# Performance work log

Hardware: AMD Instinct MI355X
Metric: run time of the kernel (lower is better)

The kernel has to match this reference:

```python
import jax, jax.numpy as jnp
import numpy as np

IN_F = 256
OUT_F = 256
ALPHA = 0.2  # LeakyReLU negative slope


def _xavier(key, shape, gain=1.414):
    fan_in, fan_out = shape[0], shape[1]
    limit = gain * np.sqrt(6.0 / (fan_in + fan_out))
    return jax.random.uniform(key, shape, jnp.float32, -limit, limit)


def setup_inputs() -> dict:
    key = jax.random.key(0)
    k1, k2, k3, k4, k5, k6 = jax.random.split(key, 6)
    B, N = 8, 2048
    h = jax.random.normal(k1, (B, N, IN_F), jnp.float32)
    adj = jax.random.randint(k2, (B, N, N), 0, 2, jnp.int32)
    lrgt1 = jax.random.normal(k3, (B, N, OUT_F), jnp.float32)
    W1 = _xavier(k4, (IN_F, IN_F))
    W2 = _xavier(k5, (OUT_F, OUT_F))
    a = _xavier(k6, (2 * IN_F, 1))
    return {"h": h, "adj": adj, "lrgt1": lrgt1, "W1": W1, "W2": W2, "a": a}


def reference(h, adj, lrgt1, W1, W2, a):
    # Wh: [B,N,in], wlrgt: [B,N,out]
    Wh = jnp.matmul(h, W1)
    wlrgt = jnp.matmul(lrgt1, W2)
    # additive attention scores: e[b,i,j] = leaky_relu(Wh_i @ a1 + Wh_j @ a2)
    a1 = a[:IN_F, 0]   # [in]
    a2 = a[IN_F:, 0]   # [in]
    Wh1 = jnp.einsum('bnc,c->bn', Wh, a1)  # [B,N]
    Wh2 = jnp.einsum('bnc,c->bn', Wh, a2)  # [B,N]
    e = jax.nn.leaky_relu(Wh1[:, :, None] + Wh2[:, None, :], ALPHA)  # [B,N,N]
    neg = jnp.float32(-9e15)
    masked = jnp.where(adj > 0, e, neg)
    attention = jax.nn.softmax(masked, axis=2)
    # dropout p=0.0 / eval mode -> identity
    h_prime = jnp.matmul(attention, Wh)      # [B,N,in]
    gt_prime = jnp.matmul(attention, wlrgt)  # [B,N,out]
    return (jax.nn.elu(h_prime), jax.nn.elu(gt_prime))
```

## Files before the change

### kernel.cpp

```cpp
#include <hip/hip_runtime.h>
#include <hip/hip_bf16.h>

#define IN_F 256
#define NN   2048
#define BB   8
#define NEGV (-9.0e15f)

typedef unsigned short u16;
typedef __attribute__((ext_vector_type(8))) short short8x;
typedef __attribute__((ext_vector_type(4))) float float4x;

__device__ __forceinline__ u16 f2b(float f) {
    union { float f; unsigned int u; } x; x.f = f;
    unsigned int r = x.u + 0x7FFFu + ((x.u >> 16) & 1u);
    return (u16)(r >> 16);
}

__device__ __forceinline__ float logitf(float wh1v, float w, int av) {
    float e = wh1v + w;
    e = (e >= 0.f) ? e : 0.2f * e;
    return (av > 0) ? e : NEGV;
}

__device__ __forceinline__ void transp_body(const float* __restrict__ src,
                                            u16* __restrict__ dst,
                                            int R, int C, int tid,
                                            float (*tile)[33])
{
    const int per = (R / 32) * (C / 32);
    const int b  = tid / per;
    const int tt = tid % per;
    const int jt = tt / (C / 32);
    const int ct = tt % (C / 32);
    src += (long)b * R * C;
    dst += (long)b * R * C;

    const int tx = threadIdx.x & 31, ty = threadIdx.x >> 5;
#pragma unroll
    for (int i = 0; i < 4; ++i)
        tile[ty + i * 8][tx] = src[(long)(jt * 32 + ty + i * 8) * C + ct * 32 + tx];
    __syncthreads();
#pragma unroll
    for (int i = 0; i < 4; ++i)
        dst[(long)(ct * 32 + ty + i * 8) * R + jt * 32 + tx] = f2b(tile[tx][ty + i * 8]);
}

__global__ __launch_bounds__(256) void prep(const float* __restrict__ h,
                                            const float* __restrict__ g,
                                            const float* __restrict__ W1,
                                            const float* __restrict__ W2,
                                            const float* __restrict__ a,
                                            u16* __restrict__ HbfT,
                                            u16* __restrict__ GbfT,
                                            u16* __restrict__ W1T,
                                            u16* __restrict__ W2T,
                                            float* __restrict__ v1,
                                            float* __restrict__ v2)
{
    __shared__ float tile[32][33];
    __shared__ float s1[IN_F], s2[IN_F];
    const int bid = blockIdx.x;

    if (bid < 4096) {
        transp_body(h, HbfT, NN, IN_F, bid, tile);
    } else if (bid < 8192) {
        transp_body(g, GbfT, NN, IN_F, bid - 4096, tile);
    } else if (bid < 8256) {
        transp_body(W1, W1T, IN_F, IN_F, bid - 8192, tile);
    } else if (bid < 8320) {
        transp_body(W2, W2T, IN_F, IN_F, bid - 8256, tile);
    } else {
        const int t = threadIdx.x;
        s1[t] = a[t];
        s2[t] = a[IN_F + t];
        __syncthreads();
        float acc1 = 0.f, acc2 = 0.f;
        for (int c = 0; c < IN_F; ++c) {
            float w = W1[t * IN_F + c];
            acc1 += w * s1[c];
            acc2 += w * s2[c];
        }
        v1[t] = acc1;
        v2[t] = acc2;
    }
}

__global__ __launch_bounds__(256) void rowdots(const float* __restrict__ h,
                                               const float* __restrict__ v1,
                                               const float* __restrict__ v2,
                                               float* __restrict__ Wh1,
                                               float* __restrict__ Wh2)
{
    const int wave = threadIdx.x >> 6;
    const int lane = threadIdx.x & 63;
    const long row = (long)blockIdx.x * 4 + wave;
    const int c0 = lane * 4;

    float4 v  = *(const float4*)(h + row * IN_F + c0);
    float4 a1 = *(const float4*)(v1 + c0);
    float4 a2 = *(const float4*)(v2 + c0);

    float s1 = v.x * a1.x + v.y * a1.y + v.z * a1.z + v.w * a1.w;
    float s2 = v.x * a2.x + v.y * a2.y + v.z * a2.z + v.w * a2.w;
#pragma unroll
    for (int off = 32; off; off >>= 1) {
        s1 += __shfl_xor(s1, off, 64);
        s2 += __shfl_xor(s2, off, 64);
    }
    if (lane == 0) { Wh1[row] = s1; Wh2[row] = s2; }
}

__global__ __launch_bounds__(512, 4) void attn_mfma(
    const int* __restrict__ adj,
    const u16* __restrict__ HbfT, const u16* __restrict__ GbfT,
    const float* __restrict__ Wh1, const float* __restrict__ Wh2,
    u16* __restrict__ PH, u16* __restrict__ PG)
{
    const int t = threadIdx.x;
    const int wave = t >> 6, lane = t & 63;
    const int b = blockIdx.x >> 6;
    const long gi0 = (long)blockIdx.x * 32;

    __shared__ __align__(16) u16 Afrag[2][4096];
    __shared__ float sred[512];
    __shared__ float ssc[33];

    const int rr = t >> 4, sg = t & 15;
    const long adjR = (gi0 + rr) * (long)NN;
    const float* wh2b = Wh2 + (long)b * NN;
    const float wh1rr = Wh1[gi0 + rr];

    {
        float4 w = *(const float4*)(wh2b + t * 4);
        sred[t] = fmaxf(fmaxf(w.x, w.y), fmaxf(w.z, w.w));
    }
    __syncthreads();
    if (t < 64) {
        float v = sred[t * 8];
#pragma unroll
        for (int k = 1; k < 8; ++k) v = fmaxf(v, sred[t * 8 + k]);
#pragma unroll
        for (int off = 32; off; off >>= 1) v = fmaxf(v, __shfl_xor(v, off, 64));
        if (t == 0) ssc[32] = v;
    }
    __syncthreads();
    const float mm = wh1rr + ssc[32];
    const float mv = (mm >= 0.f) ? mm : 0.2f * mm;

    const int ks0 = sg >> 2;
    const int wl  = (rr & 15) + ((sg & 3) << 4);
    const int prt = rr >> 4;
    const int aoff = ((ks0 * 2 + prt) * 64 + wl) * 8;

    float4x accH[2][2], accG[2][2];
#pragma unroll
    for (int rt = 0; rt < 2; ++rt)
#pragma unroll
        for (int ct = 0; ct < 2; ++ct) {
            accH[rt][ct] = (float4x)0.0f;
            accG[rt][ct] = (float4x)0.0f;
        }

    const int bn = lane & 15, bq = lane >> 4;
    const long hbase = (long)b * IN_F * NN;
    float lloc = 0.f;

    int4   a0 = *(const int4*)(adj + adjR + sg * 8);
    int4   a1 = *(const int4*)(adj + adjR + sg * 8 + 4);
    float4 w0 = *(const float4*)(wh2b + sg * 8);
    float4 w1 = *(const float4*)(wh2b + sg * 8 + 4);

    for (int kch = 0; kch < 16; ++kch) {
        const int j0 = kch * 128;

        union { short8x v; u16 u[8]; } pk;
        float p;
        p = __expf(logitf(wh1rr, w0.x, a0.x) - mv); lloc += p; pk.u[0] = f2b(p);
        p = __expf(logitf(wh1rr, w0.y, a0.y) - mv); lloc += p; pk.u[1] = f2b(p);
        p = __expf(logitf(wh1rr, w0.z, a0.z) - mv); lloc += p; pk.u[2] = f2b(p);
        p = __expf(logitf(wh1rr, w0.w, a0.w) - mv); lloc += p; pk.u[3] = f2b(p);
        p = __expf(logitf(wh1rr, w1.x, a1.x) - mv); lloc += p; pk.u[4] = f2b(p);
        p = __expf(logitf(wh1rr, w1.y, a1.y) - mv); lloc += p; pk.u[5] = f2b(p);
        p = __expf(logitf(wh1rr, w1.z, a1.z) - mv); lloc += p; pk.u[6] = f2b(p);
        p = __expf(logitf(wh1rr, w1.w, a1.w) - mv); lloc += p; pk.u[7] = f2b(p);

        if (kch < 15) {
            const long o = adjR + (kch + 1) * 128 + sg * 8;
            const int  w = (kch + 1) * 128 + sg * 8;
            a0 = *(const int4*)(adj + o);
            a1 = *(const int4*)(adj + o + 4);
            w0 = *(const float4*)(wh2b + w);
            w1 = *(const float4*)(wh2b + w + 4);
        }

        *(short8x*)&Afrag[kch & 1][aoff] = pk.v;
        __syncthreads();

        const u16* ab = Afrag[kch & 1];
#pragma unroll
        for (int ks = 0; ks < 4; ++ks) {
            short8x A0 = *(const short8x*)&ab[((ks * 2 + 0) * 64 + lane) * 8];
            short8x A1 = *(const short8x*)&ab[((ks * 2 + 1) * 64 + lane) * 8];
            const int jj = j0 + ks * 32 + bq * 8;
#pragma unroll
            for (int ct = 0; ct < 2; ++ct) {
                const int c = wave * 32 + ct * 16 + bn;
                const long bi = hbase + (long)c * NN + jj;
                short8x Bh = *(const short8x*)(HbfT + bi);
                short8x Bg = *(const short8x*)(GbfT + bi);
                accH[0][ct] = __builtin_amdgcn_mfma_f32_16x16x32_bf16(A0, Bh, accH[0][ct], 0, 0, 0);
                accH[1][ct] = __builtin_amdgcn_mfma_f32_16x16x32_bf16(A1, Bh, accH[1][ct], 0, 0, 0);
                accG[0][ct] = __builtin_amdgcn_mfma_f32_16x16x32_bf16(A0, Bg, accG[0][ct], 0, 0, 0);
                accG[1][ct] = __builtin_amdgcn_mfma_f32_16x16x32_bf16(A1, Bg, accG[1][ct], 0, 0, 0);
            }
        }
    }

    __syncthreads();
    sred[rr * 16 + sg] = lloc;
    __syncthreads();
    if (t < 32) {
        float v = sred[t * 16];
#pragma unroll
        for (int k = 1; k < 16; ++k) v += sred[t * 16 + k];
        ssc[t] = 1.0f / v;
    }
    __syncthreads();

#pragma unroll
    for (int rt = 0; rt < 2; ++rt)
#pragma unroll
        for (int ct = 0; ct < 2; ++ct) {
            const int c = wave * 32 + ct * 16 + bn;
#pragma unroll
            for (int reg = 0; reg < 4; ++reg) {
                const int rl = rt * 16 + bq * 4 + reg;
                const float il = ssc[rl];
                const long row = gi0 + rl;
                PH[row * IN_F + c] = f2b(accH[rt][ct][reg] * il);
                PG[row * IN_F + c] = f2b(accG[rt][ct][reg] * il);
            }
        }
}

__global__ __launch_bounds__(256) void epi2(const u16* __restrict__ PH,
                                            const u16* __restrict__ PG,
                                            const u16* __restrict__ W1T,
                                            const u16* __restrict__ W2T,
                                            float* __restrict__ out)
{
    int bid = blockIdx.x;
    const u16* X;
    const u16* WT;
    float* o;
    if (bid < 512) { X = PH; WT = W1T; o = out; }
    else           { X = PG; WT = W2T; o = out + (long)BB * NN * IN_F; bid -= 512; }

    const int t = threadIdx.x;
    const int wave = t >> 6, lane = t & 63;
    const long i0 = (long)bid * 32;

    __shared__ __align__(16) u16 Afrag[8 * 2 * 64 * 8];

    const int m = t >> 3, ks0 = t & 7, rt0 = m >> 4, lm = m & 15;
    const u16* xp = X + (i0 + m) * IN_F + ks0 * 32;
#pragma unroll
    for (int q = 0; q < 4; ++q) {
        short8x v = *(const short8x*)(xp + q * 8);
        *(short8x*)&Afrag[((ks0 * 2 + rt0) * 64 + lm + q * 16) * 8] = v;
    }
    __syncthreads();

    float4x acc[2][4];
#pragma unroll
    for (int rt = 0; rt < 2; ++rt)
#pragma unroll
        for (int ct = 0; ct < 4; ++ct) acc[rt][ct] = (float4x)0.0f;

    const int bn = lane & 15, bq = lane >> 4;
#pragma unroll
    for (int ks = 0; ks < 8; ++ks) {
        short8x A0 = *(const short8x*)&Afrag[((ks * 2 + 0) * 64 + lane) * 8];
        short8x A1 = *(const short8x*)&Afrag[((ks * 2 + 1) * 64 + lane) * 8];
#pragma unroll
        for (int ct = 0; ct < 4; ++ct) {
            const int n = wave * 64 + ct * 16 + bn;
            short8x Bw = *(const short8x*)(WT + n * IN_F + ks * 32 + bq * 8);
            acc[0][ct] = __builtin_amdgcn_mfma_f32_16x16x32_bf16(A0, Bw, acc[0][ct], 0, 0, 0);
            acc[1][ct] = __builtin_amdgcn_mfma_f32_16x16x32_bf16(A1, Bw, acc[1][ct], 0, 0, 0);
        }
    }

#pragma unroll
    for (int rt = 0; rt < 2; ++rt)
#pragma unroll
        for (int ct = 0; ct < 4; ++ct) {
            const int n = wave * 64 + ct * 16 + bn;
#pragma unroll
            for (int reg = 0; reg < 4; ++reg) {
                const long row = i0 + rt * 16 + bq * 4 + reg;
                float v = acc[rt][ct][reg];
                v = (v > 0.f) ? v : (__expf(v) - 1.f);
                o[row * IN_F + n] = v;
            }
        }
}

extern "C" void kernel_launch(void* const* d_in, const int* in_sizes, int n_in,
                              void* d_out, int out_size, void* d_ws, size_t ws_size,
                              hipStream_t stream)
{
    int ih = -1, ig = -1, iadj = -1, iw1 = -1, iw2 = -1, ia = -1;
    for (int i = 0; i < n_in; ++i) {
        int s = in_sizes[i];
        if      (s == BB * NN * NN)   { if (iadj < 0) iadj = i; }
        else if (s == BB * NN * IN_F) { if (ih < 0) ih = i; else if (ig < 0) ig = i; }
        else if (s == IN_F * IN_F)    { if (iw1 < 0) iw1 = i; else if (iw2 < 0) iw2 = i; }
        else if (s == 2 * IN_F)       { if (ia < 0) ia = i; }
    }
    if (ih < 0 || ig < 0 || iadj < 0 || iw1 < 0 || iw2 < 0 || ia < 0) {
        ih = 0; iadj = 1; ig = 2; iw1 = 3; iw2 = 4; ia = 5;
    }
    const float* h     = (const float*)d_in[ih];
    const int*   adj   = (const int*)  d_in[iadj];
    const float* lrgt1 = (const float*)d_in[ig];
    const float* W1    = (const float*)d_in[iw1];
    const float* W2    = (const float*)d_in[iw2];
    const float* a     = (const float*)d_in[ia];
    float* out = (float*)d_out;

    float* ws   = (float*)d_ws;
    float* v1   = ws;
    float* v2   = v1 + IN_F;
    float* Wh1  = v2 + IN_F;
    float* Wh2  = Wh1 + BB * NN;
    u16* W1T  = (u16*)(Wh2 + BB * NN);
    u16* W2T  = W1T + IN_F * IN_F;
    u16* HbfT = W2T + IN_F * IN_F;
    u16* GbfT = HbfT + (long)BB * IN_F * NN;
    u16* PH   = GbfT + (long)BB * IN_F * NN;
    u16* PG   = PH + (long)BB * NN * IN_F;

    const int nrows = BB * NN;

    prep     <<<8321,        256, 0, stream>>>(h, lrgt1, W1, W2, a,
                                               HbfT, GbfT, W1T, W2T, v1, v2);
    rowdots  <<<nrows / 4,   256, 0, stream>>>(h, v1, v2, Wh1, Wh2);
    attn_mfma<<<nrows / 32,  512, 0, stream>>>(adj, HbfT, GbfT, Wh1, Wh2, PH, PG);
    epi2     <<<2 * nrows / 32, 256, 0, stream>>>(PH, PG, W1T, W2T, out);
}
```

Measured before the change: 364.1 us.

## Software-pipeline B operand loads, swizzle block order, and lighten barrier

Register-prefetches the next k-step's B fragments (H and G, both column tiles) one step ahead so global load latency overlaps the current MFMAs. Swizzles the block index so consecutive workgroups come from different batches. Replaces __syncthreads with an explicit lgkmcnt wait plus s_barrier, so pending global prefetches are not drained at the barrier. This costs extra vector registers for the prefetched fragments, and the swizzle changes how L2 is shared between blocks.

Measured after the change: 375.6 us. 3.1% more time.

```diff
diff --git a/kernel.cpp b/kernel.cpp
--- a/kernel.cpp
+++ b/kernel.cpp
@@ -118,8 +118,9 @@
 {
     const int t = threadIdx.x;
     const int wave = t >> 6, lane = t & 63;
-    const int b = blockIdx.x >> 6;
-    const long gi0 = (long)blockIdx.x * 32;
+    const int bswz = ((blockIdx.x & 7) << 6) | (blockIdx.x >> 3);
+    const int b = bswz >> 6;
+    const long gi0 = (long)bswz * 32;
 
     __shared__ __align__(16) u16 Afrag[2][4096];
     __shared__ float sred[512];
@@ -165,10 +166,20 @@
     const long hbase = (long)b * IN_F * NN;
     float lloc = 0.f;
 
+    const u16* Hb0 = HbfT + hbase + (long)(wave * 32 + bn) * NN;
+    const u16* Hb1 = Hb0 + 16 * (long)NN;
+    const u16* Gb0 = GbfT + hbase + (long)(wave * 32 + bn) * NN;
+    const u16* Gb1 = Gb0 + 16 * (long)NN;
+
     int4   a0 = *(const int4*)(adj + adjR + sg * 8);
     int4   a1 = *(const int4*)(adj + adjR + sg * 8 + 4);
     float4 w0 = *(const float4*)(wh2b + sg * 8);
     float4 w1 = *(const float4*)(wh2b + sg * 8 + 4);
+
+    short8x Bc0 = *(const short8x*)(Hb0 + bq * 8);
+    short8x Bc1 = *(const short8x*)(Gb0 + bq * 8);
+    short8x Bc2 = *(const short8x*)(Hb1 + bq * 8);
+    short8x Bc3 = *(const short8x*)(Gb1 + bq * 8);
 
     for (int kch = 0; kch < 16; ++kch) {
         const int j0 = kch * 128;
@@ -194,25 +205,31 @@
         }
 
         *(short8x*)&Afrag[kch & 1][aoff] = pk.v;
-        __syncthreads();
+        asm volatile("s_waitcnt lgkmcnt(0)\n\ts_barrier" ::: "memory");
 
         const u16* ab = Afrag[kch & 1];
+        const int jb = j0 + bq * 8;
 #pragma unroll
         for (int ks = 0; ks < 4; ++ks) {
             short8x A0 = *(const short8x*)&ab[((ks * 2 + 0) * 64 + lane) * 8];
             short8x A1 = *(const short8x*)&ab[((ks * 2 + 1) * 64 + lane) * 8];
-            const int jj = j0 + ks * 32 + bq * 8;
-#pragma unroll
-            for (int ct = 0; ct < 2; ++ct) {
-                const int c = wave * 32 + ct * 16 + bn;
-                const long bi = hbase + (long)c * NN + jj;
-                short8x Bh = *(const short8x*)(HbfT + bi);
-                short8x Bg = *(const short8x*)(GbfT + bi);
-                accH[0][ct] = __builtin_amdgcn_mfma_f32_16x16x32_bf16(A0, Bh, accH[0][ct], 0, 0, 0);
-                accH[1][ct] = __builtin_amdgcn_mfma_f32_16x16x32_bf16(A1, Bh, accH[1][ct], 0, 0, 0);
-                accG[0][ct] = __builtin_amdgcn_mfma_f32_16x16x32_bf16(A0, Bg, accG[0][ct], 0, 0, 0);
-                accG[1][ct] = __builtin_amdgcn_mfma_f32_16x16x32_bf16(A1, Bg, accG[1][ct], 0, 0, 0);
-            }
+            const int jn = (ks < 3) ? (jb + (ks + 1) * 32)
+                                    : ((kch < 15) ? (jb + 128) : jb);
+            short8x Bn0 = *(const short8x*)(Hb0 + jn);
+            short8x Bn1 = *(const short8x*)(Gb0 + jn);
+            short8x Bn2 = *(const short8x*)(Hb1 + jn);
+            short8x Bn3 = *(const short8x*)(Gb1 + jn);
+
+            accH[0][0] = __builtin_amdgcn_mfma_f32_16x16x32_bf16(A0, Bc0, accH[0][0], 0, 0, 0);
+            accH[1][0] = __builtin_amdgcn_mfma_f32_16x16x32_bf16(A1, Bc0, accH[1][0], 0, 0, 0);
+            accG[0][0] = __builtin_amdgcn_mfma_f32_16x16x32_bf16(A0, Bc1, accG[0][0], 0, 0, 0);
+            accG[1][0] = __builtin_amdgcn_mfma_f32_16x16x32_bf16(A1, Bc1, accG[1][0], 0, 0, 0);
+            accH[0][1] = __builtin_amdgcn_mfma_f32_16x16x32_bf16(A0, Bc2, accH[0][1], 0, 0, 0);
+            accH[1][1] = __builtin_amdgcn_mfma_f32_16x16x32_bf16(A1, Bc2, accH[1][1], 0, 0, 0);
+            accG[0][1] = __builtin_amdgcn_mfma_f32_16x16x32_bf16(A0, Bc3, accG[0][1], 0, 0, 0);
+            accG[1][1] = __builtin_amdgcn_mfma_f32_16x16x32_bf16(A1, Bc3, accG[1][1], 0, 0, 0);
+
+            Bc0 = Bn0; Bc1 = Bn1; Bc2 = Bn2; Bc3 = Bn3;
         }
     }
 
```

## Enlarge attention tile to 64 rows with software-pipelined MFMA fragments

Applied to the files above, without the earlier changes.

The attention kernel now handles 64 query rows per block instead of 32, and each wave owns 64 output columns of either H or G, with a 4x4 MFMA accumulator tile. This raises reuse of the P fragments and B operand loads. A and B fragments are double-buffered in registers across k-steps, and adj/Wh2 loads are prefetched one chunk ahead. Block indices are swizzled so that neighbouring blocks spread across batches. The cost is more registers (launch bounds drop to 2 blocks per CU), fewer blocks overall, and a hand-written barrier in inline asm.

After: 309.7 us. 14.9% less time.

```diff
diff --git a/kernel.cpp b/kernel.cpp
--- a/kernel.cpp
+++ b/kernel.cpp
@@ -14,12 +14,6 @@
     union { float f; unsigned int u; } x; x.f = f;
     unsigned int r = x.u + 0x7FFFu + ((x.u >> 16) & 1u);
     return (u16)(r >> 16);
-}
-
-__device__ __forceinline__ float logitf(float wh1v, float w, int av) {
-    float e = wh1v + w;
-    e = (e >= 0.f) ? e : 0.2f * e;
-    return (av > 0) ? e : NEGV;
 }
 
 __device__ __forceinline__ void transp_body(const float* __restrict__ src,
@@ -110,7 +104,57 @@
     if (lane == 0) { Wh1[row] = s1; Wh2[row] = s2; }
 }
 
-__global__ __launch_bounds__(512, 4) void attn_mfma(
+#define KSTEP(ksv, BC, BN_, AC, AN_, do_a, jnxt)                              \
+    {                                                                         \
+        if (do_a) {                                                           \
+            _Pragma("unroll") for (int rt = 0; rt < 4; ++rt)                  \
+                AN_[rt] = *(const short8x*)&ab[(((ksv) + 1) * 4 + rt) * 512 + lane * 8]; \
+        }                                                                     \
+        _Pragma("unroll") for (int ct = 0; ct < 4; ++ct)                      \
+            BN_[ct] = *(const short8x*)(Bp + ct * 16 * NN + (jnxt));          \
+        _Pragma("unroll") for (int rt = 0; rt < 4; ++rt)                      \
+            _Pragma("unroll") for (int ct = 0; ct < 4; ++ct)                  \
+                acc[rt][ct] = __builtin_amdgcn_mfma_f32_16x16x32_bf16(AC[rt], BC[ct], acc[rt][ct], 0, 0, 0); \
+    }
+
+#define CHUNK(KCH, ADJC, W4C, ADJN, W4N)                                      \
+    {                                                                         \
+        const int j0 = (KCH) * 128;                                           \
+        if ((KCH) < 15) {                                                     \
+            const int jn0 = j0 + 128 + sg * 16;                               \
+            _Pragma("unroll") for (int u = 0; u < 4; ++u) {                   \
+                W4N[u]  = *(const float4*)(wh2b + jn0 + u * 4);               \
+                ADJN[u] = *(const int4*)(adj + adjR + jn0 + u * 4);           \
+            }                                                                 \
+        }                                                                     \
+        union { short8x v; u16 e[8]; } pk0, pk1;                              \
+        _Pragma("unroll") for (int u = 0; u < 4; ++u) {                       \
+            const float wv4[4] = {W4C[u].x, W4C[u].y, W4C[u].z, W4C[u].w};    \
+            const int   av4[4] = {ADJC[u].x, ADJC[u].y, ADJC[u].z, ADJC[u].w};\
+            _Pragma("unroll") for (int c = 0; c < 4; ++c) {                   \
+                float x = wh1rr + wv4[c];                                     \
+                float e = fmaxf(x, 0.2f * x);                                 \
+                float p = __expf(e - mv);                                     \
+                p = (av4[c] > 0) ? p : 0.0f;                                  \
+                lloc += p;                                                    \
+                u16 fv = f2b(p);                                              \
+                if (u < 2) pk0.e[u * 4 + c] = fv;                             \
+                else       pk1.e[(u - 2) * 4 + c] = fv;                       \
+            }                                                                 \
+        }                                                                     \
+        u16* ab = &Afrag[(KCH) & 1][0];                                       \
+        *(short8x*)&ab[wbase0]       = pk0.v;                                 \
+        *(short8x*)&ab[wbase0 + 128] = pk1.v;                                 \
+        asm volatile("s_waitcnt lgkmcnt(0)\n\ts_barrier" ::: "memory");       \
+        _Pragma("unroll") for (int rt = 0; rt < 4; ++rt)                      \
+            A0[rt] = *(const short8x*)&ab[rt * 512 + lane * 8];               \
+        KSTEP(0, B0, B1, A0, A1, 1, j0 + 1 * 32 + bq8)                        \
+        KSTEP(1, B1, B0, A1, A0, 1, j0 + 2 * 32 + bq8)                        \
+        KSTEP(2, B0, B1, A0, A1, 1, j0 + 3 * 32 + bq8)                        \
+        KSTEP(3, B1, B0, A1, A0, 0, (((KCH) < 15) ? (j0 + 128) : j0) + bq8)   \
+    }
+
+__global__ __launch_bounds__(512, 2) void attn_mfma(
     const int* __restrict__ adj,
     const u16* __restrict__ HbfT, const u16* __restrict__ GbfT,
     const float* __restrict__ Wh1, const float* __restrict__ Wh2,
@@ -118,14 +162,15 @@
 {
     const int t = threadIdx.x;
     const int wave = t >> 6, lane = t & 63;
-    const int b = blockIdx.x >> 6;
-    const long gi0 = (long)blockIdx.x * 32;
-
-    __shared__ __align__(16) u16 Afrag[2][4096];
+    const int bswz = ((blockIdx.x & 7) << 5) | (blockIdx.x >> 3);
+    const int b = bswz >> 5;
+    const long gi0 = (long)bswz * 64;
+
+    __shared__ __align__(16) u16 Afrag[2][8192];
     __shared__ float sred[512];
-    __shared__ float ssc[33];
-
-    const int rr = t >> 4, sg = t & 15;
+    __shared__ float ssc[65];
+
+    const int rr = t >> 3, sg = t & 7;
     const long adjR = (gi0 + rr) * (long)NN;
     const float* wh2b = Wh2 + (long)b * NN;
     const float wh1rr = Wh1[gi0 + rr];
@@ -141,104 +186,71 @@
         for (int k = 1; k < 8; ++k) v = fmaxf(v, sred[t * 8 + k]);
 #pragma unroll
         for (int off = 32; off; off >>= 1) v = fmaxf(v, __shfl_xor(v, off, 64));
-        if (t == 0) ssc[32] = v;
-    }
-    __syncthreads();
-    const float mm = wh1rr + ssc[32];
+        if (t == 0) ssc[64] = v;
+    }
+    __syncthreads();
+    const float mm = wh1rr + ssc[64];
     const float mv = (mm >= 0.f) ? mm : 0.2f * mm;
 
-    const int ks0 = sg >> 2;
-    const int wl  = (rr & 15) + ((sg & 3) << 4);
-    const int prt = rr >> 4;
-    const int aoff = ((ks0 * 2 + prt) * 64 + wl) * 8;
-
-    float4x accH[2][2], accG[2][2];
-#pragma unroll
-    for (int rt = 0; rt < 2; ++rt)
-#pragma unroll
-        for (int ct = 0; ct < 2; ++ct) {
-            accH[rt][ct] = (float4x)0.0f;
-            accG[rt][ct] = (float4x)0.0f;
-        }
-
-    const int bn = lane & 15, bq = lane >> 4;
+    const int wbase0 = ((sg >> 1) * 4 + (rr >> 4)) * 512
+                     + ((rr & 15) + 16 * (2 * (sg & 1))) * 8;
+
+    float4x acc[4][4];
+#pragma unroll
+    for (int rt = 0; rt < 4; ++rt)
+#pragma unroll
+        for (int ct = 0; ct < 4; ++ct) acc[rt][ct] = (float4x)0.0f;
+
+    const int bn = lane & 15, bq = lane >> 4, bq8 = bq * 8;
     const long hbase = (long)b * IN_F * NN;
+    const u16* Bp = ((wave < 4) ? HbfT : GbfT) + hbase
+                  + (long)((wave & 3) * 64 + bn) * NN;
+
     float lloc = 0.f;
 
-    int4   a0 = *(const int4*)(adj + adjR + sg * 8);
-    int4   a1 = *(const int4*)(adj + adjR + sg * 8 + 4);
-    float4 w0 = *(const float4*)(wh2b + sg * 8);
-    float4 w1 = *(const float4*)(wh2b + sg * 8 + 4);
-
-    for (int kch = 0; kch < 16; ++kch) {
-        const int j0 = kch * 128;
-
-        union { short8x v; u16 u[8]; } pk;
-        float p;
-        p = __expf(logitf(wh1rr, w0.x, a0.x) - mv); lloc += p; pk.u[0] = f2b(p);
-        p = __expf(logitf(wh1rr, w0.y, a0.y) - mv); lloc += p; pk.u[1] = f2b(p);
-        p = __expf(logitf(wh1rr, w0.z, a0.z) - mv); lloc += p; pk.u[2] = f2b(p);
-        p = __expf(logitf(wh1rr, w0.w, a0.w) - mv); lloc += p; pk.u[3] = f2b(p);
-        p = __expf(logitf(wh1rr, w1.x, a1.x) - mv); lloc += p; pk.u[4] = f2b(p);
-        p = __expf(logitf(wh1rr, w1.y, a1.y) - mv); lloc += p; pk.u[5] = f2b(p);
-        p = __expf(logitf(wh1rr, w1.z, a1.z) - mv); lloc += p; pk.u[6] = f2b(p);
-        p = __expf(logitf(wh1rr, w1.w, a1.w) - mv); lloc += p; pk.u[7] = f2b(p);
-
-        if (kch < 15) {
-            const long o = adjR + (kch + 1) * 128 + sg * 8;
-            const int  w = (kch + 1) * 128 + sg * 8;
-            a0 = *(const int4*)(adj + o);
-            a1 = *(const int4*)(adj + o + 4);
-            w0 = *(const float4*)(wh2b + w);
-            w1 = *(const float4*)(wh2b + w + 4);
-        }
-
-        *(short8x*)&Afrag[kch & 1][aoff] = pk.v;
-        __syncthreads();
-
-        const u16* ab = Afrag[kch & 1];
-#pragma unroll
-        for (int ks = 0; ks < 4; ++ks) {
-            short8x A0 = *(const short8x*)&ab[((ks * 2 + 0) * 64 + lane) * 8];
-            short8x A1 = *(const short8x*)&ab[((ks * 2 + 1) * 64 + lane) * 8];
-            const int jj = j0 + ks * 32 + bq * 8;
-#pragma unroll
-            for (int ct = 0; ct < 2; ++ct) {
-                const int c = wave * 32 + ct * 16 + bn;
-                const long bi = hbase + (long)c * NN + jj;
-                short8x Bh = *(const short8x*)(HbfT + bi);
-                short8x Bg = *(const short8x*)(GbfT + bi);
-                accH[0][ct] = __builtin_amdgcn_mfma_f32_16x16x32_bf16(A0, Bh, accH[0][ct], 0, 0, 0);
-                accH[1][ct] = __builtin_amdgcn_mfma_f32_16x16x32_bf16(A1, Bh, accH[1][ct], 0, 0, 0);
-                accG[0][ct] = __builtin_amdgcn_mfma_f32_16x16x32_bf16(A0, Bg, accG[0][ct], 0, 0, 0);
-                accG[1][ct] = __builtin_amdgcn_mfma_f32_16x16x32_bf16(A1, Bg, accG[1][ct], 0, 0, 0);
-            }
-        }
-    }
-
-    __syncthreads();
-    sred[rr * 16 + sg] = lloc;
-    __syncthreads();
-    if (t < 32) {
-        float v = sred[t * 16];
-#pragma unroll
-        for (int k = 1; k < 16; ++k) v += sred[t * 16 + k];
+    short8x A0[4], A1[4], B0[4], B1[4];
+    int4   adjA[4], adjB[4];
+    float4 w4A[4], w4B[4];
+
+#pragma unroll
+    for (int u = 0; u < 4; ++u) {
+        adjA[u] = *(const int4*)(adj + adjR + sg * 16 + u * 4);
+        w4A[u]  = *(const float4*)(wh2b + sg * 16 + u * 4);
+        adjB[u] = adjA[u];
+        w4B[u]  = w4A[u];
+    }
+#pragma unroll
+    for (int ct = 0; ct < 4; ++ct)
+        B0[ct] = *(const short8x*)(Bp + ct * 16 * NN + bq8);
+
+    for (int kp = 0; kp < 8; ++kp) {
+        CHUNK(kp * 2,     adjA, w4A, adjB, w4B)
+        CHUNK(kp * 2 + 1, adjB, w4B, adjA, w4A)
+    }
+
+    sred[t] = lloc;
+    __syncthreads();
+    if (t < 64) {
+        float v = sred[t * 8];
+#pragma unroll
+        for (int k = 1; k < 8; ++k) v += sred[t * 8 + k];
         ssc[t] = 1.0f / v;
     }
     __syncthreads();
 
-#pragma unroll
-    for (int rt = 0; rt < 2; ++rt)
-#pragma unroll
-        for (int ct = 0; ct < 2; ++ct) {
-            const int c = wave * 32 + ct * 16 + bn;
+    u16* dst = (wave < 4) ? PH : PG;
+    const int colb = (wave & 3) * 64;
+#pragma unroll
+    for (int rt = 0; rt < 4; ++rt)
+#pragma unroll
+        for (int ct = 0; ct < 4; ++ct) {
+            const int c = colb + ct * 16 + bn;
 #pragma unroll
             for (int reg = 0; reg < 4; ++reg) {
                 const int rl = rt * 16 + bq * 4 + reg;
                 const float il = ssc[rl];
                 const long row = gi0 + rl;
-                PH[row * IN_F + c] = f2b(accH[rt][ct][reg] * il);
-                PG[row * IN_F + c] = f2b(accG[rt][ct][reg] * il);
+                dst[row * IN_F + c] = f2b(acc[rt][ct][reg] * il);
             }
         }
 }
@@ -346,6 +358,6 @@
     prep     <<<8321,        256, 0, stream>>>(h, lrgt1, W1, W2, a,
                                                HbfT, GbfT, W1T, W2T, v1, v2);
     rowdots  <<<nrows / 4,   256, 0, stream>>>(h, v1, v2, Wh1, Wh2);
-    attn_mfma<<<nrows / 32,  512, 0, stream>>>(adj, HbfT, GbfT, Wh1, Wh2, PH, PG);
+    attn_mfma<<<nrows / 64,  512, 0, stream>>>(adj, HbfT, GbfT, Wh1, Wh2, PH, PG);
     epi2     <<<2 * nrows / 32, 256, 0, stream>>>(PH, PG, W1T, W2T, out);
 }
```
